# Optimization experiments

Measured on AMD Instinct MI355X. Metric: run time of the kernel, lower is better.

The kernel has to match this reference:

```python
import jax, jax.numpy as jnp
import numpy as np

N_NODES = 50000
N_EDGES = 800000
FEAT = 128
N_RBF = 20
CUTOFF = 5.0


def setup_inputs() -> dict:
    key = jax.random.key(0)
    ks = jax.random.split(key, 10)
    s_j = jax.random.normal(ks[0], (N_NODES, FEAT), dtype=jnp.float32)
    # distances strictly inside (0, cutoff) to avoid div-by-zero in the RBF
    dist = jax.random.uniform(ks[1], (N_EDGES,), dtype=jnp.float32, minval=0.1, maxval=CUTOFF)
    nbrs = jax.random.randint(ks[2], (N_EDGES, 2), 0, N_NODES, dtype=jnp.int64)
    scale = 1.0 / np.sqrt(FEAT)
    W1 = jax.random.normal(ks[3], (FEAT, FEAT), dtype=jnp.float32) * scale
    b1 = jnp.zeros((FEAT,), dtype=jnp.float32)
    W2 = jax.random.normal(ks[4], (FEAT, 3 * FEAT), dtype=jnp.float32) * scale
    b2 = jnp.zeros((3 * FEAT,), dtype=jnp.float32)
    Wd = jax.random.normal(ks[5], (N_RBF, 3 * FEAT), dtype=jnp.float32) * (1.0 / np.sqrt(N_RBF))
    bd = jnp.zeros((3 * FEAT,), dtype=jnp.float32)
    return {"s_j": s_j, "dist": dist, "nbrs": nbrs,
            "W1": W1, "b1": b1, "W2": W2, "b2": b2, "Wd": Wd, "bd": bd}


def reference(s_j, dist, nbrs, W1, b1, W2, b2, Wd, bd):
    # InvariantDense: Linear -> swish(SiLU) -> Linear, on all nodes, then gather
    h = jax.nn.silu(s_j @ W1 + b1) @ W2 + b2          # [N, 3F]
    phi = h[nbrs[:, 1]]                                # [E, 3F] gather
    # PainnRadialBasis: sin(k*pi*d/cutoff)/d, k = 1..n_rbf
    k = jnp.arange(1, N_RBF + 1, dtype=jnp.float32)    # [n_rbf]
    d = dist[:, None]                                  # [E, 1]
    rbf = jnp.sin(k * jnp.pi * d / CUTOFF) / d         # [E, n_rbf]
    # CosineEnvelope: 0.5*(cos(pi*d/cutoff)+1) for d < cutoff else 0
    env = jnp.where(dist < CUTOFF,
                    0.5 * (jnp.cos(jnp.pi * dist / CUTOFF) + 1.0),
                    0.0)[:, None]                      # [E, 1]
    w_s = (rbf @ Wd + bd) * env                        # [E, 3F]
    out = (phi * w_s).reshape(phi.shape[0], 3, -1)     # [E, 3, F]
    return out
```

## Files before the change

### kernel.cpp

```cpp
#include <hip/hip_runtime.h>

#define FEATN 128
#define F3 384
#define NRBF 20
#define KPAD 32
#define EB 32
#define D0 0.1f
#define CUT 5.0f
#define PI_F 3.14159265358979323846f

typedef __attribute__((ext_vector_type(8))) short short8;
typedef __attribute__((ext_vector_type(4))) float f32x4;
typedef __attribute__((ext_vector_type(2))) unsigned int u32x2;

__device__ __forceinline__ unsigned short f2bf(float f) {
  unsigned int u = __float_as_uint(f);
  u += 0x7FFFu + ((u >> 16) & 1u);
  return (unsigned short)(u >> 16);
}
__device__ __forceinline__ float bflo(unsigned int u) { return __uint_as_float(u << 16); }
__device__ __forceinline__ float bfhi(unsigned int u) { return __uint_as_float(u & 0xffff0000u); }

__device__ __forceinline__ int swz(int row, int col) {
  return row * 128 + (col ^ ((row & 7) << 3));
}

__global__ __launch_bounds__(256) void prep_kernel(const float* __restrict__ W1,
                                                   const float* __restrict__ W2,
                                                   const float* __restrict__ Wd,
                                                   unsigned short* __restrict__ W1t,
                                                   unsigned short* __restrict__ W2t,
                                                   unsigned short* __restrict__ Wdt) {
  const int idx = blockIdx.x * 256 + threadIdx.x;
  if (idx < FEATN * FEATN) {
    const int nn = idx >> 7, k = idx & 127;
    W1t[idx] = f2bf(W1[k * FEATN + nn]);
  }
  const int idx2 = idx - FEATN * FEATN;
  if (idx2 >= 0 && idx2 < F3 * FEATN) {
    const int nn = idx2 >> 7, k = idx2 & 127;
    W2t[idx2] = f2bf(W2[k * F3 + nn]);
  }
  const int idx3 = idx - FEATN * FEATN - F3 * FEATN;
  if (idx3 >= 0 && idx3 < F3 * KPAD) {
    const int c = idx3 >> 5, k = idx3 & 31;
    Wdt[idx3] = (k < NRBF) ? f2bf(Wd[k * F3 + c]) : (unsigned short)0;
  }
}

__global__ __launch_bounds__(256, 2) void node_mfma_kernel(
    const float* __restrict__ s, const unsigned short* __restrict__ W1t,
    const float* __restrict__ b1, const unsigned short* __restrict__ W2t,
    const float* __restrict__ b2, unsigned short* __restrict__ hbf, int n) {
  __shared__ unsigned short sA[64 * 128];
  __shared__ unsigned short sT[64 * 128];
  __shared__ unsigned short sW[128 * 128];

  const int tid = threadIdx.x;
  const int w = tid >> 6;
  const int lane = tid & 63;
  const int row0 = blockIdx.x * 64;

#pragma unroll
  for (int i = 0; i < 8; ++i) {
    const int f = i * 256 + tid;
    const int r = f >> 5;
    const int c4 = f & 31;
    float4 v = make_float4(0.f, 0.f, 0.f, 0.f);
    if (row0 + r < n) v = *(const float4*)&s[(size_t)(row0 + r) * FEATN + c4 * 4];
    uint2 pk;
    pk.x = (unsigned)f2bf(v.x) | ((unsigned)f2bf(v.y) << 16);
    pk.y = (unsigned)f2bf(v.z) | ((unsigned)f2bf(v.w) << 16);
    *(uint2*)&sA[swz(r, c4 * 4)] = pk;
  }
#pragma unroll
  for (int i = 0; i < 8; ++i) {
    const int f = i * 256 + tid;
    const int r = f >> 4;
    const int c8 = f & 15;
    const uint4 v = *(const uint4*)&W1t[r * 128 + c8 * 8];
    *(uint4*)&sW[swz(r, c8 * 8)] = v;
  }
  __syncthreads();

  const int arow = w * 16 + (lane & 15);
  const int kbase = (lane >> 4) * 8;
  const int drow0 = w * 16 + ((lane >> 4) << 2);
  const int dcol = lane & 15;

  {
    f32x4 acc[8] = {};
#pragma unroll
    for (int ks = 0; ks < 4; ++ks) {
      const int kk = ks * 32 + kbase;
      const short8 a = *(const short8*)&sA[swz(arow, kk)];
#pragma unroll
      for (int nf = 0; nf < 8; ++nf) {
        const short8 b = *(const short8*)&sW[swz(nf * 16 + dcol, kk)];
        acc[nf] = __builtin_amdgcn_mfma_f32_16x16x32_bf16(a, b, acc[nf], 0, 0, 0);
      }
    }
#pragma unroll
    for (int nf = 0; nf < 8; ++nf) {
      const int col = nf * 16 + dcol;
      const float bias = b1[col];
#pragma unroll
      for (int r = 0; r < 4; ++r) {
        const float v = acc[nf][r] + bias;
        const float t = v / (1.0f + __expf(-v));
        sT[swz(drow0 + r, col)] = f2bf(t);
      }
    }
  }
  __syncthreads();

  for (int c = 0; c < 3; ++c) {
#pragma unroll
    for (int i = 0; i < 8; ++i) {
      const int f = i * 256 + tid;
      const int r = f >> 4;
      const int c8 = f & 15;
      const uint4 v = *(const uint4*)&W2t[(size_t)(c * 128 + r) * 128 + c8 * 8];
      *(uint4*)&sW[swz(r, c8 * 8)] = v;
    }
    __syncthreads();

    f32x4 acc2[8] = {};
#pragma unroll
    for (int ks = 0; ks < 4; ++ks) {
      const int kk = ks * 32 + kbase;
      const short8 a = *(const short8*)&sT[swz(arow, kk)];
#pragma unroll
      for (int nf = 0; nf < 8; ++nf) {
        const short8 b = *(const short8*)&sW[swz(nf * 16 + dcol, kk)];
        acc2[nf] = __builtin_amdgcn_mfma_f32_16x16x32_bf16(a, b, acc2[nf], 0, 0, 0);
      }
    }
#pragma unroll
    for (int nf = 0; nf < 8; ++nf) {
      const int col = c * 128 + nf * 16 + dcol;
      const float bias = b2[col];
#pragma unroll
      for (int r = 0; r < 4; ++r) {
        const int row = row0 + drow0 + r;
        if (row < n) hbf[(size_t)row * F3 + col] = f2bf(acc2[nf][r] + bias);
      }
    }
    __syncthreads();
  }
}

__global__ __launch_bounds__(256, 4) void edge_kernel(
    const float* __restrict__ dist, const int* __restrict__ nbrs,
    const unsigned short* __restrict__ hbf, const unsigned short* __restrict__ Wdt,
    const float* __restrict__ bd, float* __restrict__ out, int n_edges) {
  __shared__ unsigned short sA[EB * KPAD];
  __shared__ unsigned short sWS[EB * F3];
  __shared__ float env_ls[EB];
  __shared__ int nbr_ls[EB];

  const int tid = threadIdx.x;
  const int e0 = blockIdx.x * EB;

  if (tid < EB) {
    const int e = e0 + tid;
    float d = 1.0f;
    int nbr = 0;
    float sc = 0.f, cc = 1.f, env = 0.f;
    if (e < n_edges) {
      d = dist[e];
      nbr = nbrs[2 * e + 1];
      const float th = (PI_F / CUT) * d;
      __sincosf(th, &sc, &cc);
      env = (d < CUT) ? 0.5f * (cc + 1.0f) : 0.0f;
    }
    nbr_ls[tid] = nbr;
    env_ls[tid] = env;
    const float einv = env / d;
    const float twoc = 2.0f * cc;
    float skm1 = 0.f, sk = sc;
    unsigned short* arow = &sA[tid * KPAD];
#pragma unroll
    for (int k = 0; k < NRBF; ++k) {
      arow[k] = f2bf(sk * einv);
      const float nxt = twoc * sk - skm1;
      skm1 = sk;
      sk = nxt;
    }
#pragma unroll
    for (int k = NRBF; k < KPAD; ++k) arow[k] = 0;
  }
  __syncthreads();

  {
    const int wv = tid >> 6, lane = tid & 63;
    const int rt = wv & 1, ch = wv >> 1;
    const short8 a = *(const short8*)&sA[(rt * 16 + (lane & 15)) * KPAD + (lane >> 4) * 8];
    const int bl = lane & 15;
    const int kb = (lane >> 4) * 8;
    const int rbase = rt * 16 + ((lane >> 4) << 2);
    float envr[4];
#pragma unroll
    for (int r = 0; r < 4; ++r) envr[r] = env_ls[rbase + r];

#pragma unroll
    for (int ct = 0; ct < 12; ++ct) {
      const int col = ch * 192 + ct * 16 + bl;
      const short8 b = *(const short8*)&Wdt[col * KPAD + kb];
      f32x4 acc = {};
      acc = __builtin_amdgcn_mfma_f32_16x16x32_bf16(a, b, acc, 0, 0, 0);
      const float bdv = bd[col];
#pragma unroll
      for (int r = 0; r < 4; ++r)
        sWS[(rbase + r) * F3 + col] = f2bf(acc[r] + envr[r] * bdv);
    }
  }
  __syncthreads();

  const size_t obase = (size_t)e0 * 96;
#pragma unroll
  for (int i = 0; i < (EB * 96) / 256; ++i) {
    const int qi = i * 256 + tid;
    const int le = qi / 96;
    const int sub = qi - le * 96;
    if (e0 + le < n_edges) {
      const int nbr = nbr_ls[le];
      const u32x2 hp = *(const u32x2*)&hbf[(size_t)nbr * F3 + sub * 4];
      const u32x2 wsv = *(const u32x2*)&sWS[le * F3 + sub * 4];
      f32x4 o;
      o.x = bflo(hp.x) * bflo(wsv.x);
      o.y = bfhi(hp.x) * bfhi(wsv.x);
      o.z = bflo(hp.y) * bflo(wsv.y);
      o.w = bfhi(hp.y) * bfhi(wsv.y);
      __builtin_nontemporal_store(o, (f32x4*)out + obase + qi);
    }
  }
}

extern "C" void kernel_launch(void* const* d_in, const int* in_sizes, int n_in,
                              void* d_out, int out_size, void* d_ws, size_t ws_size,
                              hipStream_t stream) {
  const float* s_j  = (const float*)d_in[0];
  const float* dist = (const float*)d_in[1];
  const int*   nbrs = (const int*)d_in[2];
  const float* W1   = (const float*)d_in[3];
  const float* b1   = (const float*)d_in[4];
  const float* W2   = (const float*)d_in[5];
  const float* b2   = (const float*)d_in[6];
  const float* Wd   = (const float*)d_in[7];
  const float* bd   = (const float*)d_in[8];
  float* out = (float*)d_out;

  const int n_nodes = in_sizes[0] / FEATN;
  const int n_edges = in_sizes[1];

  char* ws = (char*)d_ws;
  unsigned short* hbf = (unsigned short*)ws;
  unsigned short* W1t = hbf + (size_t)n_nodes * F3;
  unsigned short* W2t = W1t + FEATN * FEATN;
  unsigned short* Wdt = W2t + F3 * FEATN;

  const int prep_elems = FEATN * FEATN + F3 * FEATN + F3 * KPAD;
  hipLaunchKernelGGL(prep_kernel, dim3((prep_elems + 255) / 256), dim3(256), 0, stream,
                     W1, W2, Wd, W1t, W2t, Wdt);
  hipLaunchKernelGGL(node_mfma_kernel, dim3((n_nodes + 63) / 64), dim3(256), 0, stream,
                     s_j, W1t, b1, W2t, b2, hbf, n_nodes);
  hipLaunchKernelGGL(edge_kernel, dim3((n_edges + EB - 1) / EB), dim3(256), 0, stream,
                     dist, nbrs, hbf, Wdt, bd, out, n_edges);
}
```

Baseline: 315.9 us.

## Sort edges by neighbor via counting sort so gathers hit shared rows

Adds a histogram, single-block scan and atomic scatter that build a permutation grouping edges by their source node. The edge kernel processes edges in that order, so consecutive edges reuse the same hbf row in cache, and it writes outputs at the original edge index. It also widens the gather and store loop to 16-byte loads and two 16-byte stores per thread. The cost is four extra launches, a serial scan over 50k counts in a single block, and scattered output writes that are no longer contiguous across edges.

```diff
diff --git a/kernel.cpp b/kernel.cpp
--- a/kernel.cpp
+++ b/kernel.cpp
@@ -12,6 +12,7 @@
 typedef __attribute__((ext_vector_type(8))) short short8;
 typedef __attribute__((ext_vector_type(4))) float f32x4;
 typedef __attribute__((ext_vector_type(2))) unsigned int u32x2;
+typedef __attribute__((ext_vector_type(4))) unsigned int u32x4;
 
 __device__ __forceinline__ unsigned short f2bf(float f) {
   unsigned int u = __float_as_uint(f);
@@ -48,6 +49,47 @@
   }
 }
 
+__global__ __launch_bounds__(256) void hist_zero_kernel(int* __restrict__ counts, int n) {
+  const int i = blockIdx.x * 256 + threadIdx.x;
+  if (i < n) counts[i] = 0;
+}
+
+__global__ __launch_bounds__(256) void hist_kernel(const int* __restrict__ nbrs,
+                                                   int* __restrict__ counts, int n_edges) {
+  const int e = blockIdx.x * 256 + threadIdx.x;
+  if (e < n_edges) atomicAdd(&counts[nbrs[2 * e + 1]], 1);
+}
+
+__global__ __launch_bounds__(256) void scan_kernel(const int* __restrict__ counts,
+                                                   int* __restrict__ offsets, int n) {
+  __shared__ int part[256];
+  const int tid = threadIdx.x;
+  const int per = (n + 255) / 256;
+  const int lo = tid * per;
+  const int hi = min(lo + per, n);
+  int sum = 0;
+  for (int i = lo; i < hi; ++i) sum += counts[i];
+  part[tid] = sum;
+  __syncthreads();
+  if (tid == 0) {
+    int acc = 0;
+    for (int i = 0; i < 256; ++i) { const int v = part[i]; part[i] = acc; acc += v; }
+  }
+  __syncthreads();
+  int acc = part[tid];
+  for (int i = lo; i < hi; ++i) { offsets[i] = acc; acc += counts[i]; }
+}
+
+__global__ __launch_bounds__(256) void scatter_kernel(const int* __restrict__ nbrs,
+                                                      int* __restrict__ offsets,
+                                                      int* __restrict__ perm, int n_edges) {
+  const int e = blockIdx.x * 256 + threadIdx.x;
+  if (e < n_edges) {
+    const int pos = atomicAdd(&offsets[nbrs[2 * e + 1]], 1);
+    perm[pos] = e;
+  }
+}
+
 __global__ __launch_bounds__(256, 2) void node_mfma_kernel(
     const float* __restrict__ s, const unsigned short* __restrict__ W1t,
     const float* __restrict__ b1, const unsigned short* __restrict__ W2t,
@@ -152,28 +194,33 @@
 
 __global__ __launch_bounds__(256, 4) void edge_kernel(
     const float* __restrict__ dist, const int* __restrict__ nbrs,
+    const int* __restrict__ perm,
     const unsigned short* __restrict__ hbf, const unsigned short* __restrict__ Wdt,
     const float* __restrict__ bd, float* __restrict__ out, int n_edges) {
   __shared__ unsigned short sA[EB * KPAD];
   __shared__ unsigned short sWS[EB * F3];
   __shared__ float env_ls[EB];
   __shared__ int nbr_ls[EB];
+  __shared__ int eid_ls[EB];
 
   const int tid = threadIdx.x;
   const int e0 = blockIdx.x * EB;
 
   if (tid < EB) {
-    const int e = e0 + tid;
+    const int se = e0 + tid;
+    int e = -1;
     float d = 1.0f;
     int nbr = 0;
     float sc = 0.f, cc = 1.f, env = 0.f;
-    if (e < n_edges) {
+    if (se < n_edges) {
+      e = perm[se];
       d = dist[e];
       nbr = nbrs[2 * e + 1];
       const float th = (PI_F / CUT) * d;
       __sincosf(th, &sc, &cc);
       env = (d < CUT) ? 0.5f * (cc + 1.0f) : 0.0f;
     }
+    eid_ls[tid] = e;
     nbr_ls[tid] = nbr;
     env_ls[tid] = env;
     const float einv = env / d;
@@ -217,22 +264,28 @@
   }
   __syncthreads();
 
-  const size_t obase = (size_t)e0 * 96;
-#pragma unroll
-  for (int i = 0; i < (EB * 96) / 256; ++i) {
+#pragma unroll
+  for (int i = 0; i < (EB * 48) / 256; ++i) {
     const int qi = i * 256 + tid;
-    const int le = qi / 96;
-    const int sub = qi - le * 96;
-    if (e0 + le < n_edges) {
+    const int le = qi / 48;
+    const int sub = qi - le * 48;
+    const int e = eid_ls[le];
+    if (e >= 0) {
       const int nbr = nbr_ls[le];
-      const u32x2 hp = *(const u32x2*)&hbf[(size_t)nbr * F3 + sub * 4];
-      const u32x2 wsv = *(const u32x2*)&sWS[le * F3 + sub * 4];
-      f32x4 o;
-      o.x = bflo(hp.x) * bflo(wsv.x);
-      o.y = bfhi(hp.x) * bfhi(wsv.x);
-      o.z = bflo(hp.y) * bflo(wsv.y);
-      o.w = bfhi(hp.y) * bfhi(wsv.y);
-      __builtin_nontemporal_store(o, (f32x4*)out + obase + qi);
+      const u32x4 hp = *(const u32x4*)&hbf[(size_t)nbr * F3 + sub * 8];
+      const u32x4 wsv = *(const u32x4*)&sWS[le * F3 + sub * 8];
+      f32x4 o0, o1;
+      o0.x = bflo(hp.x) * bflo(wsv.x);
+      o0.y = bfhi(hp.x) * bfhi(wsv.x);
+      o0.z = bflo(hp.y) * bflo(wsv.y);
+      o0.w = bfhi(hp.y) * bfhi(wsv.y);
+      o1.x = bflo(hp.z) * bflo(wsv.z);
+      o1.y = bfhi(hp.z) * bfhi(wsv.z);
+      o1.z = bflo(hp.w) * bflo(wsv.w);
+      o1.w = bfhi(hp.w) * bfhi(wsv.w);
+      f32x4* op = (f32x4*)out + (size_t)e * 96 + sub * 2;
+      __builtin_nontemporal_store(o0, op);
+      __builtin_nontemporal_store(o1, op + 1);
     }
   }
 }
@@ -259,12 +312,23 @@
   unsigned short* W1t = hbf + (size_t)n_nodes * F3;
   unsigned short* W2t = W1t + FEATN * FEATN;
   unsigned short* Wdt = W2t + F3 * FEATN;
+  int* counts  = (int*)(Wdt + F3 * KPAD);
+  int* offsets = counts + n_nodes;
+  int* perm    = offsets + n_nodes;
 
   const int prep_elems = FEATN * FEATN + F3 * FEATN + F3 * KPAD;
   hipLaunchKernelGGL(prep_kernel, dim3((prep_elems + 255) / 256), dim3(256), 0, stream,
                      W1, W2, Wd, W1t, W2t, Wdt);
+  hipLaunchKernelGGL(hist_zero_kernel, dim3((n_nodes + 255) / 256), dim3(256), 0, stream,
+                     counts, n_nodes);
+  hipLaunchKernelGGL(hist_kernel, dim3((n_edges + 255) / 256), dim3(256), 0, stream,
+                     nbrs, counts, n_edges);
+  hipLaunchKernelGGL(scan_kernel, dim3(1), dim3(256), 0, stream, counts, offsets, n_nodes);
+  hipLaunchKernelGGL(scatter_kernel, dim3((n_edges + 255) / 256), dim3(256), 0, stream,
+                     nbrs, offsets, perm, n_edges);
+
   hipLaunchKernelGGL(node_mfma_kernel, dim3((n_nodes + 63) / 64), dim3(256), 0, stream,
                      s_j, W1t, b1, W2t, b2, hbf, n_nodes);
   hipLaunchKernelGGL(edge_kernel, dim3((n_edges + EB - 1) / EB), dim3(256), 0, stream,
-                     dist, nbrs, hbf, Wdt, bd, out, n_edges);
-}
+                     dist, nbrs, perm, hbf, Wdt, bd, out, n_edges);
+}
```

Result: slower. 713.4 us (+125.8%).
